# Optimization experiments

Measured on AMD Instinct MI355X. Metric: run time of the kernel, lower is better.

The kernel has to match this reference:

```python
import jax, jax.numpy as jnp
import numpy as np
from jax import lax

N = 5000
C = 81  # num_classes including background at index 0
BG_OFFSET = 1


def _iou_matrix(b):
    # b: [N,4] as x1,y1,x2,y2 -> pairwise IoU [N,N]
    x1, y1, x2, y2 = b[:, 0], b[:, 1], b[:, 2], b[:, 3]
    area = (x2 - x1) * (y2 - y1)  # [N]
    ix1 = jnp.maximum(x1[:, None], x1[None, :])
    iy1 = jnp.maximum(y1[:, None], y1[None, :])
    ix2 = jnp.minimum(x2[:, None], x2[None, :])
    iy2 = jnp.minimum(y2[:, None], y2[None, :])
    iw = jnp.maximum(ix2 - ix1, 0.0)
    ih = jnp.maximum(iy2 - iy1, 0.0)
    inter = iw * ih
    return inter / (area[:, None] + area[None, :] - inter)


def setup_inputs() -> dict:
    key = jax.random.key(0)
    k1, k2, k3 = jax.random.split(key, 3)
    # valid boxes: x1<x2, y1<y2 on a ~1024px canvas, size ~up to 256px
    xy1 = jax.random.uniform(k1, (N, 2), dtype=jnp.float32) * 1024.0
    wh = jax.random.uniform(k2, (N, 2), dtype=jnp.float32) * 256.0 + 1.0
    bboxes = jnp.concatenate([xy1, xy1 + wh], axis=1)  # [N,4]
    scores = jax.random.uniform(k3, (N, C), dtype=jnp.float32)  # [N,C]
    return {
        "bboxes": bboxes,
        "scores": scores,
        "conf_thresh": 0.6,
        "nms_thresh": 0.5,
        "max_instances": 300,
    }


def _multiclass_nms(bboxes, scores, conf_thresh, nms_thresh, max_instances):
    n = bboxes.shape[0]
    neg_inf = jnp.finfo(scores.dtype).min
    iou = _iou_matrix(bboxes)  # [N,N]

    def nms_one_class(score_c):  # score_c: [N]
        valid = score_c > conf_thresh
        masked = jnp.where(valid, score_c, neg_inf)
        order = jnp.argsort(masked)[::-1]  # descending score

        def step(suppressed, idx):
            keep = valid[idx] & ~suppressed[idx]
            new_sup = jnp.where(keep, suppressed | (iou[idx] > nms_thresh), suppressed)
            return new_sup, keep

        _, keeps = lax.scan(step, jnp.zeros((n,), bool), order)
        # scatter keep flags back to original box order
        return jnp.zeros((n,), bool).at[order].set(keeps)

    fg_scores = scores[:, BG_OFFSET:].T  # [C-1, N]
    keep = jax.vmap(nms_one_class)(fg_scores)  # [C-1, N]

    # global top-k over all (class, box) kept detections, sorted by score desc
    flat = jnp.where(keep, fg_scores, neg_inf).reshape(-1)  # [(C-1)*N]
    top_scores, top_idx = lax.top_k(flat, max_instances)
    cls = top_idx // n + BG_OFFSET  # [K]
    box = top_idx % n  # [K]
    valid_out = top_scores > neg_inf / 2

    sel_score = scores[box, cls]  # differentiable gather
    preds = jnp.concatenate([bboxes[box], sel_score[:, None]], axis=1)  # [K,5]
    preds = jnp.where(valid_out[:, None], preds, 0.0)
    labels = jnp.where(valid_out, cls, -1)
    return preds, labels


def reference(bboxes, scores, conf_thresh, nms_thresh, max_instances):
    return _multiclass_nms(bboxes, scores, conf_thresh, nms_thresh, max_instances)
```

## Files before the change

### kernel.cpp

```cpp
#include <hip/hip_runtime.h>

typedef unsigned long long u64;
typedef unsigned int u32;
typedef unsigned short u16;

#define MSORT 4096
#define TPB1  1024
#define TPBF  1024
#define BOXCAP 3648
#define KCAP  3072
#define RSLOT_W 10
#define KPC   300
#define SELCAP 1024
#define PREFR 64

#define WG_SCOPE __HIP_MEMORY_SCOPE_WORKGROUP

__device__ __forceinline__ float boxArea(float4 b) {
    return __fmul_rn(__fsub_rn(b.z, b.x), __fsub_rn(b.w, b.y));
}

template<bool GE>
__device__ __forceinline__ bool iou_gt(float4 a, float area_a, float4 b, float area_b, double B) {
    float ix1 = fmaxf(a.x, b.x), iy1 = fmaxf(a.y, b.y);
    float ix2 = fminf(a.z, b.z), iy2 = fminf(a.w, b.w);
    float iw  = fmaxf(__fsub_rn(ix2, ix1), 0.0f);
    float ih  = fmaxf(__fsub_rn(iy2, iy1), 0.0f);
    float inter = __fmul_rn(iw, ih);
    float uni   = __fsub_rn(__fadd_rn(area_a, area_b), inter);
    return GE ? ((double)inter >= B * (double)uni) : ((double)inter > B * (double)uni);
}

__device__ __forceinline__ int scoreBin(u32 bits) {
    int b = (int)(bits >> 12) - 0x3F000;
    return b < 0 ? 0 : (b > 2047 ? 2047 : b);
}

template<bool GE>
__device__ __forceinline__ int prefix_nms_w0(
    const float* __restrict__ bboxes, const u64* __restrict__ sorted,
    int R, double B, int tid, int c, int N, u64* __restrict__ gkept_c)
{
    u64 key = (tid < R) ? sorted[tid] : 0;
    float4 bx = make_float4(0.f, 0.f, 0.f, 0.f);
    if (tid < R) bx = ((const float4*)bboxes)[(u32)key];
    float ar = boxArea(bx);
    u64 supB = (R >= 64) ? 0ull : (~0ull << R);
    int nk = 0;
    int i = -1;
    for (;;) {
        u64 mask = (i >= 63) ? 0ull : (~0ull << (i + 1));
        u64 alive = ~supB & mask;
        if (!alive) break;
        i = (int)__builtin_ctzll(alive);
        float4 bi;
        bi.x = __shfl(bx.x, i, 64); bi.y = __shfl(bx.y, i, 64);
        bi.z = __shfl(bx.z, i, 64); bi.w = __shfl(bx.w, i, 64);
        float ai = boxArea(bi);
        if (tid == 0) {
            u64 ki = sorted[i];
            u32 flat = (u32)c * (u32)N + (u32)ki;
            gkept_c[nk] = (ki & 0xFFFFFFFF00000000ull) | (u32)(~flat);
        }
        nk++;
        bool sup = (tid > i) && iou_gt<GE>(bi, ai, bx, ar, B);
        supB |= __ballot(sup);
    }
    return nk;
}

__global__ __launch_bounds__(TPB1, 1) void nms_select_kernel(
    const float* __restrict__ bboxes, const float* __restrict__ scores,
    const float* __restrict__ conf_ptr, const float* __restrict__ nms_ptr,
    int N, int C, u64* __restrict__ gkept,
    u32* __restrict__ gK, u32* __restrict__ g65, u32* __restrict__ gPre)
{
    __shared__ u64 keys[KCAP];
    __shared__ u32 hist[2048];
    __shared__ u64 keybuf[256];
    __shared__ u64 sorted[66];
    __shared__ int chunk[64];
    __shared__ int cntS, ncollS, bstarS, nkS;

    const int tid = threadIdx.x;
    const int c   = blockIdx.x;
    const int cls = c + 1;
    const float conf = *conf_ptr;
    const float nmsT = *nms_ptr;

    for (int b = tid; b < 2048; b += TPB1) hist[b] = 0;
    if (tid < 66) sorted[tid] = 0;
    if (tid == 0) { cntS = 0; ncollS = 0; nkS = 0; }
    __syncthreads();

    for (int i = tid; i < N; i += TPB1) {
        float s = scores[(size_t)i * C + cls];
        if (s > conf) {
            int p = atomicAdd(&cntS, 1);
            if (p < KCAP) keys[p] = ((u64)__float_as_uint(s) << 32) | (u32)i;
            atomicAdd(&hist[scoreBin(__float_as_uint(s))], 1u);
        }
    }
    __syncthreads();
    const int K = cntS;
    const bool preOv = (K > KCAP);
    const int target = K < (PREFR + 1) ? K : (PREFR + 1);

    if (tid < 64) {
        int s = 0;
        #pragma unroll
        for (int b = 0; b < 32; b++) s += (int)hist[tid * 32 + b];
        chunk[tid] = s;
    }
    __syncthreads();
    if (tid == 0) {
        int acc = 0, ch = 63;
        for (; ch >= 0; ch--) { if (acc + chunk[ch] >= target) break; acc += chunk[ch]; }
        int bs = 0;
        if (ch >= 0) {
            int b = (ch << 5) + 31;
            for (; b >= (ch << 5); b--) { acc += (int)hist[b]; if (acc >= target) break; }
            bs = (b < (ch << 5)) ? (ch << 5) : b;
        }
        bstarS = bs;
    }
    __syncthreads();
    const u32 tbits = (bstarS == 0) ? 0u : (((u32)bstarS + 0x3F000u) << 12);

    const int KL = K < KCAP ? K : KCAP;
    for (int p = tid; p < KL; p += TPB1) {
        u64 k = keys[p];
        if ((u32)(k >> 32) >= tbits) {
            int pos = atomicAdd(&ncollS, 1);
            if (pos < 256) keybuf[pos] = k;
        }
    }
    __syncthreads();
    const int ncoll = ncollS;
    const bool pre = preOv || (ncoll > 256);
    for (int p = ncoll + tid; p < 256; p += TPB1) keybuf[p] = 0;
    __syncthreads();

    u64* gkept_c = gkept + (size_t)c * KPC;
    if (!pre) {
        if (tid < 256) {
            u64 my = keybuf[tid];
            int rank = 0;
            for (int j = 0; j < 256; j++) rank += (keybuf[j] > my);
            if (my && rank < PREFR + 1) sorted[rank] = my;
        }
        __syncthreads();
        const u32 tb = __float_as_uint(nmsT);
        const float Tn = __uint_as_float(tb + 1u);
        const double B = ((double)nmsT + (double)Tn) * 0.5;
        const bool geCmp = (((tb + 1u) & 1u) == 0u);
        if (tid < 64) {
            int R = ncoll < PREFR ? ncoll : PREFR;
            int nk = geCmp ? prefix_nms_w0<true >(bboxes, sorted, R, B, tid, c, N, gkept_c)
                           : prefix_nms_w0<false>(bboxes, sorted, R, B, tid, c, N, gkept_c);
            if (tid == 0) nkS = nk;
        }
        __syncthreads();
        for (int p = nkS + tid; p < KPC; p += TPB1) gkept_c[p] = 0;
    } else {
        for (int p = tid; p < KPC; p += TPB1) gkept_c[p] = 0;
    }
    if (tid == 0) {
        gK[c]   = (u32)K;
        g65[c]  = pre ? 0xFFFFFFFFu : ((ncoll >= PREFR + 1) ? (u32)(sorted[PREFR] >> 32) : 0u);
        gPre[c] = pre ? 1u : 0u;
    }
}

__global__ __launch_bounds__(1024) void nms_theta_kernel(
    const u64* __restrict__ gkept, const u32* __restrict__ gK,
    const u32* __restrict__ g65, const u32* __restrict__ gPre,
    int nc, int Mout, u32* __restrict__ gCtl)
{
    __shared__ u32 hist[2048];
    __shared__ int chunk[64];
    __shared__ u32 thetaS;
    const int tid = threadIdx.x;
    const int total = nc * KPC;
    for (int b = tid; b < 2048; b += 1024) hist[b] = 0;
    __syncthreads();
    for (int t = tid; t < total; t += 1024) {
        u64 k = gkept[t];
        if (k) atomicAdd(&hist[scoreBin((u32)(k >> 32))], 1u);
    }
    __syncthreads();
    if (tid < 64) {
        int s = 0;
        #pragma unroll
        for (int b = 0; b < 32; b++) s += (int)hist[tid * 32 + b];
        chunk[tid] = s;
    }
    __syncthreads();
    if (tid == 0) {
        int tot = 0;
        for (int ch = 0; ch < 64; ch++) tot += chunk[ch];
        u32 theta = 0u;
        if (tot >= Mout) {
            int acc = 0, ch = 63;
            for (; ch >= 0; ch--) { if (acc + chunk[ch] >= Mout) break; acc += chunk[ch]; }
            int b = (ch << 5) + 31;
            for (; b >= (ch << 5); b--) { acc += (int)hist[b]; if (acc >= Mout) break; }
            int bs = (b < (ch << 5)) ? (ch << 5) : b;
            theta = (bs <= 0) ? 0u : (((u32)bs + 0x3F000u) << 12);
        }
        gCtl[0] = theta;
        thetaS  = theta;
    }
    __syncthreads();
    const u32 theta = thetaS;
    for (int c2 = tid; c2 < nc; c2 += 1024) {
        u32 need = gPre[c2];
        if (gK[c2] > PREFR && g65[c2] >= theta) need = 1u;
        gCtl[1 + c2] = need;
    }
}

template<bool GE>
__device__ __forceinline__ u64 sweep_own(
    float4 bi, float area_i, const float4 (&breg)[RSLOT_W],
    const float (&areaj)[RSLOT_W], const float4* __restrict__ boxesLds,
    int base, int nslots, int lane, double B)
{
    u64 ns = 0;
    #pragma unroll
    for (int t = 0; t < RSLOT_W; t++)
        ns |= ((u64)iou_gt<GE>(bi, area_i, breg[t], areaj[t], B)) << (base + t);
    for (int t = RSLOT_W; t < nslots; t++) {
        float4 bj = boxesLds[((base + t) << 6) | lane];
        ns |= ((u64)iou_gt<GE>(bi, area_i, bj, boxArea(bj), B)) << (base + t);
    }
    return ns;
}

template<bool GE>
__device__ __forceinline__ int greedy_full(
    const float4* __restrict__ boxesLds, u16* __restrict__ keptR,
    float4* __restrict__ pubBox, u32* __restrict__ ctl,
    const u32* __restrict__ gsi_c, const float* __restrict__ scores,
    int cls, int C, u32 thetaBits,
    int K, int smax, double B, int lane, int wave)
{
    const int SW   = (smax + 3) >> 2;
    const int base = (wave * SW < smax) ? wave * SW : smax;
    const int end  = (base + SW < smax) ? base + SW : smax;
    const int nslots = end - base;

    float4 breg[RSLOT_W];
    float  areaj[RSLOT_W];
    #pragma unroll
    for (int t = 0; t < RSLOT_W; t++) {
        float4 b = boxesLds[((base + t) << 6) | lane];
        breg[t] = b;
        areaj[t] = boxArea(b);
    }

    u64 sup;
    {
        int t = (lane < K) ? ((K - lane + 63) >> 6) : 0;
        sup = (t >= 64) ? 0ull : (~0ull << t);
    }

    u32 seen = 0;
    if (wave != 0) {
        for (;;) {
            u32 d  = __hip_atomic_load(&ctl[2], __ATOMIC_ACQUIRE, WG_SCOPE);
            u32 cn = __hip_atomic_load(&ctl[0], __ATOMIC_ACQUIRE, WG_SCOPE);
            bool prog = (seen < cn);
            while (seen < cn) {
                float4 bi = pubBox[seen]; seen++;
                sup |= sweep_own<GE>(bi, boxArea(bi), breg, areaj, boxesLds, base, nslots, lane, B);
            }
            if (d) return -1;
            u32 aw = __hip_atomic_load(&ctl[1], __ATOMIC_ACQUIRE, WG_SCOPE);
            if (aw == (u32)wave) {
                u32 cn2 = __hip_atomic_load(&ctl[0], __ATOMIC_ACQUIRE, WG_SCOPE);
                while (seen < cn2) {
                    float4 bi = pubBox[seen]; seen++;
                    sup |= sweep_own<GE>(bi, boxArea(bi), breg, areaj, boxesLds, base, nslots, lane, B);
                }
                break;
            }
            if (!prog) __builtin_amdgcn_s_sleep(1);
        }
    }

    u32 nk = seen;
    const u32 seen0 = seen;
    int scur = base - 1;
    float4 bcur = make_float4(0.f, 0.f, 0.f, 0.f);
    float  acur = 0.f;
    int js = base << 6;

    for (;;) {
        int s = js >> 6;
        while (s > scur) {
            scur++;
            if (scur < end) {
                bcur = boxesLds[(scur << 6) | lane];
                acur = boxArea(bcur);
                u64 bit = 0;
                for (u32 k = seen0; k < nk; k++) {
                    float4 bk = pubBox[k];
                    bit |= ((u64)iou_gt<GE>(bk, boxArea(bk), bcur, acur, B));
                }
                sup |= bit << scur;
            }
        }
        if (scur >= end) {
            if (wave == 3) {
                if (lane == 0) __hip_atomic_store(&ctl[2], 1u, __ATOMIC_RELEASE, WG_SCOPE);
                return (int)nk;
            }
            if (lane == 0) __hip_atomic_store(&ctl[1], (u32)(wave + 1), __ATOMIC_RELEASE, WG_SCOPE);
            return -1;
        }
        u64 bal = __ballot((int)(((~sup) >> scur) & 1ull)) & (~0ull << (js & 63));
        if (bal == 0) { js = (scur + 1) << 6; continue; }
        int i = (scur << 6) + (int)__builtin_ctzll(bal);

        if (thetaBits) {
            u32 idx = gsi_c[i];
            float sc = scores[(size_t)idx * C + cls];
            if (__float_as_uint(sc) < thetaBits) {
                if (lane == 0) __hip_atomic_store(&ctl[2], 1u, __ATOMIC_RELEASE, WG_SCOPE);
                return (int)nk;
            }
        }
        float4 bi = boxesLds[i];
        if (lane == 0) { pubBox[nk] = bi; keptR[nk] = (u16)i; }
        nk++;
        if (nk >= KPC) {
            if (lane == 0) {
                __hip_atomic_store(&ctl[0], nk, __ATOMIC_RELEASE, WG_SCOPE);
                __hip_atomic_store(&ctl[2], 1u, __ATOMIC_RELEASE, WG_SCOPE);
            }
            return (int)nk;
        }
        if (lane == 0) __hip_atomic_store(&ctl[0], nk, __ATOMIC_RELEASE, WG_SCOPE);
        sup |= ((u64)iou_gt<GE>(bi, boxArea(bi), bcur, acur, B)) << scur;
        js = i + 1;
    }
}

__global__ __launch_bounds__(TPBF, 1) void nms_full_kernel(
    const float* __restrict__ bboxes, const float* __restrict__ scores,
    const float* __restrict__ conf_ptr, const float* __restrict__ nms_ptr,
    int N, int C, const u32* __restrict__ gCtl,
    u32* __restrict__ gsi, u64* __restrict__ gkept)
{
    const int c = blockIdx.x;
    if (gCtl[1 + c] == 0u) return;

    __shared__ __align__(16) char smem[63856];
    u64*    sortbuf  = (u64*)smem;
    float4* boxesLds = (float4*)smem;
    u16*    keptR    = (u16*)(smem + 58368);
    u32*    ctl      = (u32*)(smem + 58976);
    float4* pubBox   = (float4*)(smem + 58992);
    __shared__ int cntS;

    const int tid = threadIdx.x;
    const int cls = c + 1;
    const float conf = *conf_ptr;
    const float nmsT = *nms_ptr;
    const u32 thetaBits = gCtl[0];

    if (tid == 0) cntS = 0;
    __syncthreads();
    for (int i = tid; i < N; i += TPBF) {
        float s = scores[(size_t)i * C + cls];
        if (s > conf) {
            int p = atomicAdd(&cntS, 1);
            if (p < MSORT) sortbuf[p] = ((u64)__float_as_uint(s) << 32) | (u32)i;
        }
    }
    __syncthreads();
    int K = cntS; if (K > BOXCAP) K = BOXCAP;
    int M = 64; while (M < K) M <<= 1;
    for (int p = K + tid; p < M; p += TPBF) sortbuf[p] = 0;
    __syncthreads();
    for (int kk = 2; kk <= M; kk <<= 1) {
        for (int j = kk >> 1; j > 0; j >>= 1) {
            for (int i = tid; i < M; i += TPBF) {
                int ixj = i ^ j;
                if (ixj > i) {
                    u64 a = sortbuf[i], b = sortbuf[ixj];
                    if (((i & kk) == 0) ? (a < b) : (a > b)) { sortbuf[i] = b; sortbuf[ixj] = a; }
                }
            }
            __syncthreads();
        }
    }
    u32 myIdx[MSORT / TPBF];
    #pragma unroll
    for (int t = 0; t < MSORT / TPBF; t++) myIdx[t] = (u32)sortbuf[t * TPBF + tid];
    __syncthreads();
    u32* gsi_c = gsi + (size_t)c * BOXCAP;
    #pragma unroll
    for (int t = 0; t < MSORT / TPBF; t++) {
        int r = t * TPBF + tid;
        if (r < K) {
            u32 idx = myIdx[t];
            gsi_c[r] = idx;
            boxesLds[r] = ((const float4*)bboxes)[idx];
        }
    }
    if (tid == 0) { ctl[0] = 0; ctl[1] = 0; ctl[2] = 0; }
    __syncthreads();
    if (tid >= 256) return;

    const int lane = tid & 63;
    const int wave = tid >> 6;
    const u32 tb = __float_as_uint(nmsT);
    const float Tn = __uint_as_float(tb + 1u);
    const double B = ((double)nmsT + (double)Tn) * 0.5;
    const bool geCmp = (((tb + 1u) & 1u) == 0u);
    const int smax = (K + 63) >> 6;

    int ret = geCmp ? greedy_full<true >(boxesLds, keptR, pubBox, ctl, gsi_c, scores, cls, C, thetaBits, K, smax, B, lane, wave)
                    : greedy_full<false>(boxesLds, keptR, pubBox, ctl, gsi_c, scores, cls, C, thetaBits, K, smax, B, lane, wave);
    if (ret >= 0) {
        int kept = ret; if (kept > KPC) kept = KPC;
        u64* gkept_c = gkept + (size_t)c * KPC;
        for (int p = lane; p < kept; p += 64) {
            int rank = keptR[p];
            u32 idx = gsi_c[rank];
            float sc = scores[(size_t)idx * C + cls];
            u32 flat = (u32)c * (u32)N + idx;
            gkept_c[p] = ((u64)__float_as_uint(sc) << 32) | (u32)(~flat);
        }
        for (int p = kept + lane; p < KPC; p += 64) gkept_c[p] = 0;
    }
}

__global__ __launch_bounds__(1024) void nms_topk_kernel(
    const float* __restrict__ bboxes, const u64* __restrict__ gkept,
    int N, int nc, int Mout, float* __restrict__ out)
{
    __shared__ u32 hist[2048];
    __shared__ int chunk[64];
    __shared__ int selCount;
    __shared__ int bstarS;
    __shared__ u64 sel[SELCAP];

    const int tid = threadIdx.x;
    const int total = nc * KPC;

    for (int b = tid; b < 2048; b += 1024) hist[b] = 0;
    if (tid == 0) selCount = 0;
    __syncthreads();

    for (int t = tid; t < total; t += 1024) {
        u64 k = gkept[t];
        if (k) atomicAdd(&hist[scoreBin((u32)(k >> 32))], 1u);
    }
    __syncthreads();

    if (tid < 64) {
        int s = 0;
        #pragma unroll
        for (int b = 0; b < 32; b++) s += (int)hist[tid * 32 + b];
        chunk[tid] = s;
    }
    __syncthreads();

    if (tid == 0) {
        int acc = 0, ch = 63;
        for (; ch >= 0; ch--) {
            if (acc + chunk[ch] >= Mout) break;
            acc += chunk[ch];
        }
        int bs = 0;
        if (ch >= 0) {
            int b = (ch << 5) + 31;
            for (; b >= (ch << 5); b--) { acc += (int)hist[b]; if (acc >= Mout) break; }
            bs = (b < (ch << 5)) ? (ch << 5) : b;
        }
        bstarS = bs;
    }
    __syncthreads();
    const int bstar = bstarS;

    for (int t = tid; t < total; t += 1024) {
        u64 k = gkept[t];
        if (k && scoreBin((u32)(k >> 32)) >= bstar) {
            int p = atomicAdd(&selCount, 1);
            if (p < SELCAP) sel[p] = k;
        }
    }
    __syncthreads();
    int cnt = selCount; if (cnt > SELCAP) cnt = SELCAP;
    int SM = 512; while (SM < cnt) SM <<= 1;
    for (int p = cnt + tid; p < SM; p += 1024) sel[p] = 0;
    __syncthreads();

    for (int kk = 2; kk <= SM; kk <<= 1) {
        for (int j = kk >> 1; j > 0; j >>= 1) {
            for (int i = tid; i < SM; i += 1024) {
                int ixj = i ^ j;
                if (ixj > i) {
                    u64 a = sel[i], b = sel[ixj];
                    if (((i & kk) == 0) ? (a < b) : (a > b)) { sel[i] = b; sel[ixj] = a; }
                }
            }
            __syncthreads();
        }
    }

    for (int t = tid; t < Mout; t += 1024) {
        u64 k = (t < SM) ? sel[t] : 0;
        float px1 = 0.f, py1 = 0.f, px2 = 0.f, py2 = 0.f, ps = 0.f, plab = -1.0f;
        if (k) {
            float s  = __uint_as_float((u32)(k >> 32));
            u32 flat = ~((u32)k);
            int cc   = (int)(flat / (u32)N);
            int box  = (int)(flat - (u32)cc * (u32)N);
            float4 bb = ((const float4*)bboxes)[box];
            px1 = bb.x; py1 = bb.y; px2 = bb.z; py2 = bb.w; ps = s;
            plab = (float)(cc + 1);
        }
        out[t * 5 + 0] = px1;
        out[t * 5 + 1] = py1;
        out[t * 5 + 2] = px2;
        out[t * 5 + 3] = py2;
        out[t * 5 + 4] = ps;
        out[Mout * 5 + t] = plab;
    }
}

extern "C" void kernel_launch(void* const* d_in, const int* in_sizes, int n_in,
                              void* d_out, int out_size, void* d_ws, size_t ws_size,
                              hipStream_t stream) {
    const float* bboxes = (const float*)d_in[0];
    const float* scores = (const float*)d_in[1];
    const float* conf   = (const float*)d_in[2];
    const float* nmsT   = (const float*)d_in[3];

    const int N    = in_sizes[0] / 4;
    const int C    = in_sizes[1] / N;
    const int nc   = C - 1;
    const int Mout = out_size / 6;

    char* wsb = (char*)d_ws;
    size_t off = 0;
    u32* gsi   = (u32*)(wsb + off); off += (size_t)nc * BOXCAP * sizeof(u32);
    u64* gkept = (u64*)(wsb + off); off += (size_t)nc * KPC * sizeof(u64);
    u32* gK    = (u32*)(wsb + off); off += (size_t)((nc + 1) & ~1) * sizeof(u32);
    u32* g65   = (u32*)(wsb + off); off += (size_t)((nc + 1) & ~1) * sizeof(u32);
    u32* gPre  = (u32*)(wsb + off); off += (size_t)((nc + 1) & ~1) * sizeof(u32);
    u32* gCtl  = (u32*)(wsb + off);

    nms_select_kernel<<<nc, TPB1, 0, stream>>>(bboxes, scores, conf, nmsT, N, C, gkept, gK, g65, gPre);
    nms_theta_kernel<<<1, 1024, 0, stream>>>(gkept, gK, g65, gPre, nc, Mout, gCtl);
    nms_full_kernel<<<nc, TPBF, 0, stream>>>(bboxes, scores, conf, nmsT, N, C, gCtl, gsi, gkept);
    nms_topk_kernel<<<1, 1024, 0, stream>>>(bboxes, gkept, N, nc, Mout, (float*)d_out);
}
```

Before: 118.3 us.

## Fuse theta and top-k single-block kernels into preceding grids via last-block-done counters

```diff
diff --git a/kernel.cpp b/kernel.cpp
--- a/kernel.cpp
+++ b/kernel.cpp
@@ -14,7 +14,8 @@
 #define SELCAP 1024
 #define PREFR 64
 
-#define WG_SCOPE __HIP_MEMORY_SCOPE_WORKGROUP
+#define WG_SCOPE  __HIP_MEMORY_SCOPE_WORKGROUP
+#define DEV_SCOPE __HIP_MEMORY_SCOPE_AGENT
 
 __device__ __forceinline__ float boxArea(float4 b) {
     return __fmul_rn(__fsub_rn(b.z, b.x), __fsub_rn(b.w, b.y));
@@ -36,10 +37,44 @@
     return b < 0 ? 0 : (b > 2047 ? 2047 : b);
 }
 
+__device__ __forceinline__ void bstar_wave0(
+    const u32* __restrict__ hist, int target, int tid,
+    int* __restrict__ outBs, int* __restrict__ outTot)
+{
+    if (tid < 64) {
+        int s = 0;
+        #pragma unroll
+        for (int b = 0; b < 32; b++)
+            s += (int)hist[(tid << 5) + ((b + tid) & 31)];
+        #pragma unroll
+        for (int d = 1; d < 64; d <<= 1) {
+            int v = __shfl_down(s, d, 64);
+            if (tid + d < 64) s += v;
+        }
+        u64 bal = __ballot(s >= target);
+        int ch  = bal ? (63 - __builtin_clzll(bal)) : -1;
+        int tot = __shfl(s, 0, 64);
+        int bs  = 0;
+        if (ch >= 0) {
+            int accAbove = (ch < 63) ? __shfl(s, ch + 1, 64) : 0;
+            int h = (tid < 32) ? (int)hist[(ch << 5) + tid] : 0;
+            #pragma unroll
+            for (int d = 1; d < 32; d <<= 1) {
+                int v = __shfl_down(h, d, 64);
+                if (tid + d < 32) h += v;
+            }
+            u64 bal2 = __ballot((tid < 32) && (accAbove + h >= target));
+            bs = (ch << 5) + (63 - __builtin_clzll(bal2));
+        }
+        if (tid == 0) { *outBs = bs; if (outTot) *outTot = tot; }
+    }
+}
+
 template<bool GE>
 __device__ __forceinline__ int prefix_nms_w0(
     const float* __restrict__ bboxes, const u64* __restrict__ sorted,
-    int R, double B, int tid, int c, int N, u64* __restrict__ gkept_c)
+    int R, double B, int tid, int c, int N, u64* __restrict__ gkept_c,
+    u32* __restrict__ gHist)
 {
     u64 key = (tid < R) ? sorted[tid] : 0;
     float4 bx = make_float4(0.f, 0.f, 0.f, 0.f);
@@ -66,6 +101,8 @@
         bool sup = (tid > i) && iou_gt<GE>(bi, ai, bx, ar, B);
         supB |= __ballot(sup);
     }
+    if (tid < R && !((supB >> tid) & 1ull))
+        atomicAdd(&gHist[scoreBin((u32)(key >> 32))], 1u);
     return nk;
 }
 
@@ -73,14 +110,15 @@
     const float* __restrict__ bboxes, const float* __restrict__ scores,
     const float* __restrict__ conf_ptr, const float* __restrict__ nms_ptr,
     int N, int C, u64* __restrict__ gkept,
-    u32* __restrict__ gK, u32* __restrict__ g65, u32* __restrict__ gPre)
+    u32* __restrict__ gK, u32* __restrict__ g65, u32* __restrict__ gPre,
+    u32* __restrict__ gHist, u32* __restrict__ gCtl, u32* __restrict__ gDone,
+    int Mout)
 {
     __shared__ u64 keys[KCAP];
     __shared__ u32 hist[2048];
     __shared__ u64 keybuf[256];
     __shared__ u64 sorted[66];
-    __shared__ int chunk[64];
-    __shared__ int cntS, ncollS, bstarS, nkS;
+    __shared__ int cntS, ncollS, bstarS, nkS, lastS, thBs, thTot;
 
     const int tid = threadIdx.x;
     const int c   = blockIdx.x;
@@ -106,24 +144,7 @@
     const bool preOv = (K > KCAP);
     const int target = K < (PREFR + 1) ? K : (PREFR + 1);
 
-    if (tid < 64) {
-        int s = 0;
-        #pragma unroll
-        for (int b = 0; b < 32; b++) s += (int)hist[tid * 32 + b];
-        chunk[tid] = s;
-    }
-    __syncthreads();
-    if (tid == 0) {
-        int acc = 0, ch = 63;
-        for (; ch >= 0; ch--) { if (acc + chunk[ch] >= target) break; acc += chunk[ch]; }
-        int bs = 0;
-        if (ch >= 0) {
-            int b = (ch << 5) + 31;
-            for (; b >= (ch << 5); b--) { acc += (int)hist[b]; if (acc >= target) break; }
-            bs = (b < (ch << 5)) ? (ch << 5) : b;
-        }
-        bstarS = bs;
-    }
+    bstar_wave0(hist, target, tid, &bstarS, nullptr);
     __syncthreads();
     const u32 tbits = (bstarS == 0) ? 0u : (((u32)bstarS + 0x3F000u) << 12);
 
@@ -156,8 +177,8 @@
         const bool geCmp = (((tb + 1u) & 1u) == 0u);
         if (tid < 64) {
             int R = ncoll < PREFR ? ncoll : PREFR;
-            int nk = geCmp ? prefix_nms_w0<true >(bboxes, sorted, R, B, tid, c, N, gkept_c)
-                           : prefix_nms_w0<false>(bboxes, sorted, R, B, tid, c, N, gkept_c);
+            int nk = geCmp ? prefix_nms_w0<true >(bboxes, sorted, R, B, tid, c, N, gkept_c, gHist)
+                           : prefix_nms_w0<false>(bboxes, sorted, R, B, tid, c, N, gkept_c, gHist);
             if (tid == 0) nkS = nk;
         }
         __syncthreads();
@@ -170,50 +191,24 @@
         g65[c]  = pre ? 0xFFFFFFFFu : ((ncoll >= PREFR + 1) ? (u32)(sorted[PREFR] >> 32) : 0u);
         gPre[c] = pre ? 1u : 0u;
     }
-}
-
-__global__ __launch_bounds__(1024) void nms_theta_kernel(
-    const u64* __restrict__ gkept, const u32* __restrict__ gK,
-    const u32* __restrict__ g65, const u32* __restrict__ gPre,
-    int nc, int Mout, u32* __restrict__ gCtl)
-{
-    __shared__ u32 hist[2048];
-    __shared__ int chunk[64];
-    __shared__ u32 thetaS;
-    const int tid = threadIdx.x;
-    const int total = nc * KPC;
-    for (int b = tid; b < 2048; b += 1024) hist[b] = 0;
-    __syncthreads();
-    for (int t = tid; t < total; t += 1024) {
-        u64 k = gkept[t];
-        if (k) atomicAdd(&hist[scoreBin((u32)(k >> 32))], 1u);
-    }
-    __syncthreads();
-    if (tid < 64) {
-        int s = 0;
-        #pragma unroll
-        for (int b = 0; b < 32; b++) s += (int)hist[tid * 32 + b];
-        chunk[tid] = s;
-    }
-    __syncthreads();
-    if (tid == 0) {
-        int tot = 0;
-        for (int ch = 0; ch < 64; ch++) tot += chunk[ch];
-        u32 theta = 0u;
-        if (tot >= Mout) {
-            int acc = 0, ch = 63;
-            for (; ch >= 0; ch--) { if (acc + chunk[ch] >= Mout) break; acc += chunk[ch]; }
-            int b = (ch << 5) + 31;
-            for (; b >= (ch << 5); b--) { acc += (int)hist[b]; if (acc >= Mout) break; }
-            int bs = (b < (ch << 5)) ? (ch << 5) : b;
-            theta = (bs <= 0) ? 0u : (((u32)bs + 0x3F000u) << 12);
-        }
-        gCtl[0] = theta;
-        thetaS  = theta;
-    }
-    __syncthreads();
-    const u32 theta = thetaS;
-    for (int c2 = tid; c2 < nc; c2 += 1024) {
+
+    __syncthreads();
+    if (tid == 0)
+        lastS = (__hip_atomic_fetch_add(gDone, 1u, __ATOMIC_ACQ_REL, DEV_SCOPE)
+                 == (u32)(gridDim.x - 1)) ? 1 : 0;
+    __syncthreads();
+    if (!lastS) return;
+    __threadfence();
+
+    for (int b = tid; b < 2048; b += TPB1) hist[b] = gHist[b];
+    __syncthreads();
+    bstar_wave0(hist, Mout, tid, &thBs, &thTot);
+    __syncthreads();
+    u32 theta = 0u;
+    if (thTot >= Mout && thBs > 0) theta = (((u32)thBs + 0x3F000u) << 12);
+    if (tid == 0) gCtl[0] = theta;
+    const int nclass = (int)gridDim.x;
+    for (int c2 = tid; c2 < nclass; c2 += TPB1) {
         u32 need = gPre[c2];
         if (gK[c2] > PREFR && g65[c2] >= theta) need = 1u;
         gCtl[1 + c2] = need;
@@ -347,161 +342,142 @@
     }
 }
 
-__global__ __launch_bounds__(TPBF, 1) void nms_full_kernel(
+__global__ __launch_bounds__(TPBF, 1) void nms_full_topk_kernel(
     const float* __restrict__ bboxes, const float* __restrict__ scores,
     const float* __restrict__ conf_ptr, const float* __restrict__ nms_ptr,
     int N, int C, const u32* __restrict__ gCtl,
-    u32* __restrict__ gsi, u64* __restrict__ gkept)
+    u32* __restrict__ gsi, u64* __restrict__ gkept,
+    int Mout, float* __restrict__ out, u32* __restrict__ gDone)
 {
+    __shared__ __align__(16) char smem[63856];
+    __shared__ int cntS, lastS, selCountS, bs4S;
+
     const int c = blockIdx.x;
-    if (gCtl[1 + c] == 0u) return;
-
-    __shared__ __align__(16) char smem[63856];
-    u64*    sortbuf  = (u64*)smem;
-    float4* boxesLds = (float4*)smem;
-    u16*    keptR    = (u16*)(smem + 58368);
-    u32*    ctl      = (u32*)(smem + 58976);
-    float4* pubBox   = (float4*)(smem + 58992);
-    __shared__ int cntS;
-
     const int tid = threadIdx.x;
-    const int cls = c + 1;
-    const float conf = *conf_ptr;
-    const float nmsT = *nms_ptr;
-    const u32 thetaBits = gCtl[0];
-
-    if (tid == 0) cntS = 0;
-    __syncthreads();
-    for (int i = tid; i < N; i += TPBF) {
-        float s = scores[(size_t)i * C + cls];
-        if (s > conf) {
-            int p = atomicAdd(&cntS, 1);
-            if (p < MSORT) sortbuf[p] = ((u64)__float_as_uint(s) << 32) | (u32)i;
-        }
-    }
-    __syncthreads();
-    int K = cntS; if (K > BOXCAP) K = BOXCAP;
-    int M = 64; while (M < K) M <<= 1;
-    for (int p = K + tid; p < M; p += TPBF) sortbuf[p] = 0;
-    __syncthreads();
-    for (int kk = 2; kk <= M; kk <<= 1) {
-        for (int j = kk >> 1; j > 0; j >>= 1) {
-            for (int i = tid; i < M; i += TPBF) {
-                int ixj = i ^ j;
-                if (ixj > i) {
-                    u64 a = sortbuf[i], b = sortbuf[ixj];
-                    if (((i & kk) == 0) ? (a < b) : (a > b)) { sortbuf[i] = b; sortbuf[ixj] = a; }
+
+    if (gCtl[1 + c] != 0u) {
+        u64*    sortbuf  = (u64*)smem;
+        float4* boxesLds = (float4*)smem;
+        u16*    keptR    = (u16*)(smem + 58368);
+        u32*    ctl      = (u32*)(smem + 58976);
+        float4* pubBox   = (float4*)(smem + 58992);
+
+        const int cls = c + 1;
+        const float conf = *conf_ptr;
+        const float nmsT = *nms_ptr;
+        const u32 thetaBits = gCtl[0];
+
+        if (tid == 0) cntS = 0;
+        __syncthreads();
+        for (int i = tid; i < N; i += TPBF) {
+            float s = scores[(size_t)i * C + cls];
+            if (s > conf) {
+                int p = atomicAdd(&cntS, 1);
+                if (p < MSORT) sortbuf[p] = ((u64)__float_as_uint(s) << 32) | (u32)i;
+            }
+        }
+        __syncthreads();
+        int K = cntS; if (K > BOXCAP) K = BOXCAP;
+        int M = 64; while (M < K) M <<= 1;
+        for (int p = K + tid; p < M; p += TPBF) sortbuf[p] = 0;
+        __syncthreads();
+        for (int kk = 2; kk <= M; kk <<= 1) {
+            for (int j = kk >> 1; j > 0; j >>= 1) {
+                for (int i = tid; i < M; i += TPBF) {
+                    int ixj = i ^ j;
+                    if (ixj > i) {
+                        u64 a = sortbuf[i], b = sortbuf[ixj];
+                        if (((i & kk) == 0) ? (a < b) : (a > b)) { sortbuf[i] = b; sortbuf[ixj] = a; }
+                    }
                 }
-            }
-            __syncthreads();
-        }
-    }
-    u32 myIdx[MSORT / TPBF];
-    #pragma unroll
-    for (int t = 0; t < MSORT / TPBF; t++) myIdx[t] = (u32)sortbuf[t * TPBF + tid];
-    __syncthreads();
-    u32* gsi_c = gsi + (size_t)c * BOXCAP;
-    #pragma unroll
-    for (int t = 0; t < MSORT / TPBF; t++) {
-        int r = t * TPBF + tid;
-        if (r < K) {
-            u32 idx = myIdx[t];
-            gsi_c[r] = idx;
-            boxesLds[r] = ((const float4*)bboxes)[idx];
-        }
-    }
-    if (tid == 0) { ctl[0] = 0; ctl[1] = 0; ctl[2] = 0; }
-    __syncthreads();
-    if (tid >= 256) return;
-
-    const int lane = tid & 63;
-    const int wave = tid >> 6;
-    const u32 tb = __float_as_uint(nmsT);
-    const float Tn = __uint_as_float(tb + 1u);
-    const double B = ((double)nmsT + (double)Tn) * 0.5;
-    const bool geCmp = (((tb + 1u) & 1u) == 0u);
-    const int smax = (K + 63) >> 6;
-
-    int ret = geCmp ? greedy_full<true >(boxesLds, keptR, pubBox, ctl, gsi_c, scores, cls, C, thetaBits, K, smax, B, lane, wave)
-                    : greedy_full<false>(boxesLds, keptR, pubBox, ctl, gsi_c, scores, cls, C, thetaBits, K, smax, B, lane, wave);
-    if (ret >= 0) {
-        int kept = ret; if (kept > KPC) kept = KPC;
-        u64* gkept_c = gkept + (size_t)c * KPC;
-        for (int p = lane; p < kept; p += 64) {
-            int rank = keptR[p];
-            u32 idx = gsi_c[rank];
-            float sc = scores[(size_t)idx * C + cls];
-            u32 flat = (u32)c * (u32)N + idx;
-            gkept_c[p] = ((u64)__float_as_uint(sc) << 32) | (u32)(~flat);
-        }
-        for (int p = kept + lane; p < KPC; p += 64) gkept_c[p] = 0;
-    }
-}
-
-__global__ __launch_bounds__(1024) void nms_topk_kernel(
-    const float* __restrict__ bboxes, const u64* __restrict__ gkept,
-    int N, int nc, int Mout, float* __restrict__ out)
-{
-    __shared__ u32 hist[2048];
-    __shared__ int chunk[64];
-    __shared__ int selCount;
-    __shared__ int bstarS;
-    __shared__ u64 sel[SELCAP];
-
-    const int tid = threadIdx.x;
-    const int total = nc * KPC;
-
-    for (int b = tid; b < 2048; b += 1024) hist[b] = 0;
-    if (tid == 0) selCount = 0;
-    __syncthreads();
-
-    for (int t = tid; t < total; t += 1024) {
+                __syncthreads();
+            }
+        }
+        u32 myIdx[MSORT / TPBF];
+        #pragma unroll
+        for (int t = 0; t < MSORT / TPBF; t++) myIdx[t] = (u32)sortbuf[t * TPBF + tid];
+        __syncthreads();
+        u32* gsi_c = gsi + (size_t)c * BOXCAP;
+        #pragma unroll
+        for (int t = 0; t < MSORT / TPBF; t++) {
+            int r = t * TPBF + tid;
+            if (r < K) {
+                u32 idx = myIdx[t];
+                gsi_c[r] = idx;
+                boxesLds[r] = ((const float4*)bboxes)[idx];
+            }
+        }
+        if (tid == 0) { ctl[0] = 0; ctl[1] = 0; ctl[2] = 0; }
+        __syncthreads();
+
+        if (tid < 256) {
+            const int lane = tid & 63;
+            const int wave = tid >> 6;
+            const u32 tb = __float_as_uint(nmsT);
+            const float Tn = __uint_as_float(tb + 1u);
+            const double B = ((double)nmsT + (double)Tn) * 0.5;
+            const bool geCmp = (((tb + 1u) & 1u) == 0u);
+            const int smax = (K + 63) >> 6;
+
+            int ret = geCmp ? greedy_full<true >(boxesLds, keptR, pubBox, ctl, gsi_c, scores, cls, C, thetaBits, K, smax, B, lane, wave)
+                            : greedy_full<false>(boxesLds, keptR, pubBox, ctl, gsi_c, scores, cls, C, thetaBits, K, smax, B, lane, wave);
+            if (ret >= 0) {
+                int kept = ret; if (kept > KPC) kept = KPC;
+                u64* gkept_c = gkept + (size_t)c * KPC;
+                for (int p = lane; p < kept; p += 64) {
+                    int rank = keptR[p];
+                    u32 idx = gsi_c[rank];
+                    float sc = scores[(size_t)idx * C + cls];
+                    u32 flat = (u32)c * (u32)N + idx;
+                    gkept_c[p] = ((u64)__float_as_uint(sc) << 32) | (u32)(~flat);
+                }
+                for (int p = kept + lane; p < KPC; p += 64) gkept_c[p] = 0;
+            }
+        }
+    }
+
+    __syncthreads();
+    if (tid == 0)
+        lastS = (__hip_atomic_fetch_add(gDone, 1u, __ATOMIC_ACQ_REL, DEV_SCOPE)
+                 == (u32)(gridDim.x - 1)) ? 1 : 0;
+    __syncthreads();
+    if (!lastS) return;
+    __threadfence();
+
+    u64* sel   = (u64*)smem;
+    u32* hist4 = (u32*)(smem + 8192);
+    const int total = (int)gridDim.x * KPC;
+
+    for (int b = tid; b < 2048; b += TPBF) hist4[b] = 0;
+    if (tid == 0) selCountS = 0;
+    __syncthreads();
+
+    for (int t = tid; t < total; t += TPBF) {
         u64 k = gkept[t];
-        if (k) atomicAdd(&hist[scoreBin((u32)(k >> 32))], 1u);
-    }
-    __syncthreads();
-
-    if (tid < 64) {
-        int s = 0;
-        #pragma unroll
-        for (int b = 0; b < 32; b++) s += (int)hist[tid * 32 + b];
-        chunk[tid] = s;
-    }
-    __syncthreads();
-
-    if (tid == 0) {
-        int acc = 0, ch = 63;
-        for (; ch >= 0; ch--) {
-            if (acc + chunk[ch] >= Mout) break;
-            acc += chunk[ch];
-        }
-        int bs = 0;
-        if (ch >= 0) {
-            int b = (ch << 5) + 31;
-            for (; b >= (ch << 5); b--) { acc += (int)hist[b]; if (acc >= Mout) break; }
-            bs = (b < (ch << 5)) ? (ch << 5) : b;
-        }
-        bstarS = bs;
-    }
-    __syncthreads();
-    const int bstar = bstarS;
-
-    for (int t = tid; t < total; t += 1024) {
+        if (k) atomicAdd(&hist4[scoreBin((u32)(k >> 32))], 1u);
+    }
+    __syncthreads();
+
+    bstar_wave0(hist4, Mout, tid, &bs4S, nullptr);
+    __syncthreads();
+    const int bstar = bs4S;
+
+    for (int t = tid; t < total; t += TPBF) {
         u64 k = gkept[t];
         if (k && scoreBin((u32)(k >> 32)) >= bstar) {
-            int p = atomicAdd(&selCount, 1);
+            int p = atomicAdd(&selCountS, 1);
             if (p < SELCAP) sel[p] = k;
         }
     }
     __syncthreads();
-    int cnt = selCount; if (cnt > SELCAP) cnt = SELCAP;
+    int cnt = selCountS; if (cnt > SELCAP) cnt = SELCAP;
     int SM = 512; while (SM < cnt) SM <<= 1;
-    for (int p = cnt + tid; p < SM; p += 1024) sel[p] = 0;
+    for (int p = cnt + tid; p < SM; p += TPBF) sel[p] = 0;
     __syncthreads();
 
     for (int kk = 2; kk <= SM; kk <<= 1) {
         for (int j = kk >> 1; j > 0; j >>= 1) {
-            for (int i = tid; i < SM; i += 1024) {
+            for (int i = tid; i < SM; i += TPBF) {
                 int ixj = i ^ j;
                 if (ixj > i) {
                     u64 a = sel[i], b = sel[ixj];
@@ -512,7 +488,7 @@
         }
     }
 
-    for (int t = tid; t < Mout; t += 1024) {
+    for (int t = tid; t < Mout; t += TPBF) {
         u64 k = (t < SM) ? sel[t] : 0;
         float px1 = 0.f, py1 = 0.f, px2 = 0.f, py2 = 0.f, ps = 0.f, plab = -1.0f;
         if (k) {
@@ -553,10 +529,16 @@
     u32* gK    = (u32*)(wsb + off); off += (size_t)((nc + 1) & ~1) * sizeof(u32);
     u32* g65   = (u32*)(wsb + off); off += (size_t)((nc + 1) & ~1) * sizeof(u32);
     u32* gPre  = (u32*)(wsb + off); off += (size_t)((nc + 1) & ~1) * sizeof(u32);
-    u32* gCtl  = (u32*)(wsb + off);
-
-    nms_select_kernel<<<nc, TPB1, 0, stream>>>(bboxes, scores, conf, nmsT, N, C, gkept, gK, g65, gPre);
-    nms_theta_kernel<<<1, 1024, 0, stream>>>(gkept, gK, g65, gPre, nc, Mout, gCtl);
-    nms_full_kernel<<<nc, TPBF, 0, stream>>>(bboxes, scores, conf, nmsT, N, C, gCtl, gsi, gkept);
-    nms_topk_kernel<<<1, 1024, 0, stream>>>(bboxes, gkept, N, nc, Mout, (float*)d_out);
-}
+    u32* gCtl  = (u32*)(wsb + off); off += (size_t)((1 + nc + 1) & ~1) * sizeof(u32);
+    u32* gHist = (u32*)(wsb + off); off += 2048 * sizeof(u32);
+    u32* gDone = (u32*)(wsb + off); off += 2 * sizeof(u32);
+
+    hipMemsetAsync(gHist, 0, (2048 + 2) * sizeof(u32), stream);
+
+    nms_select_kernel<<<nc, TPB1, 0, stream>>>(bboxes, scores, conf, nmsT, N, C,
+                                               gkept, gK, g65, gPre, gHist, gCtl,
+                                               gDone, Mout);
+    nms_full_topk_kernel<<<nc, TPBF, 0, stream>>>(bboxes, scores, conf, nmsT, N, C,
+                                                  gCtl, gsi, gkept, Mout,
+                                                  (float*)d_out, gDone + 1);
+}
```

New measurement: 134.4 us. 1.14x slower.
